# Optimization experiments

Measured on AMD Instinct MI355X. Metric: run time of the kernel, lower is better.

The kernel has to match this reference:

```python
import jax, jax.numpy as jnp
import numpy as np

N_HEAD = 8
D_HEAD = 64
HIDDEN = 512
T = 2048
BS = 4
SCALE = D_HEAD ** -0.5


def setup_inputs() -> dict:
    key = jax.random.key(0)
    k1, k2, k3 = jax.random.split(key, 3)
    x = jax.random.normal(k1, (BS, T, HIDDEN), dtype=jnp.float32)
    # torch Linear weight is (out,in); we store as (in,out) for x @ W
    W_qkv = jax.random.normal(k2, (HIDDEN, (2 * N_HEAD + 1) * D_HEAD), dtype=jnp.float32) * 0.02
    W_out = jax.random.normal(k3, (D_HEAD, HIDDEN), dtype=jnp.float32) * 0.02
    return {"x": x, "W_qkv": W_qkv, "W_out": W_out}


def reference(x, W_qkv, W_out):
    bs, t, h = x.shape
    qkv = x @ W_qkv  # (bs, t, (2H+1)*d)
    q, k, v = jnp.split(qkv, [N_HEAD * D_HEAD, 2 * N_HEAD * D_HEAD], axis=-1)
    q = q.reshape(bs, t, N_HEAD, D_HEAD)
    k = k.reshape(bs, t, N_HEAD, D_HEAD)
    # v is shared across heads: (bs, t, d)
    score = jnp.einsum("bqhd,bkhd->bhqk", q, k) * SCALE
    causal = jnp.triu(jnp.full((t, t), -jnp.inf, dtype=score.dtype), 1)
    score = score + causal[None, None, :, :]
    prob = jax.nn.softmax(score, axis=-1)  # (bs, H, t, t)
    attn_vec = jnp.einsum("bhqk,bkd->bhqd", prob, v)  # shared V broadcast over heads
    m_attn_vec = jnp.mean(attn_vec, axis=1)  # head-mean: (bs, t, d)
    out = m_attn_vec @ W_out  # (bs, t, hidden)
    return out, attn_vec
```

## Files before the change

kernel.cpp:

```cpp
#include <hip/hip_runtime.h>
#include <hip/hip_bf16.h>

#define NHEAD  8
#define DHEAD  64
#define HIDDEN 512
#define SEQ_T  2048
#define BATCH  4
#define NQKV   1088
#define QPITCH 1152
#define NT     32
#define NROWS  (BATCH * SEQ_T)
#define NBH    (BATCH * NHEAD)
#define QSC    (0.125f * 1.44269504f)

typedef __attribute__((ext_vector_type(8))) short short8;
typedef __attribute__((ext_vector_type(4))) float f32x4;

__device__ __forceinline__ unsigned short f2bf(float f) {
  unsigned int u = __float_as_uint(f);
  u += 0x7FFFu + ((u >> 16) & 1u);
  return (unsigned short)(u >> 16);
}
__device__ __forceinline__ float bf2f(unsigned short u) {
  return __uint_as_float((unsigned int)u << 16);
}

__device__ __forceinline__ void load_lds16(const unsigned short* g, unsigned short* l) {
  __builtin_amdgcn_global_load_lds((const __attribute__((address_space(1))) void*)g,
                                   (__attribute__((address_space(3))) void*)l, 16, 0, 0);
}

__global__ __launch_bounds__(256) void prep(const float* __restrict__ x,
                                            const float* __restrict__ W,
                                            const float* __restrict__ Wout,
                                            unsigned short* __restrict__ xb,
                                            unsigned short* __restrict__ Wt,
                                            unsigned short* __restrict__ Wob) {
  const int bx = blockIdx.x;
  const int tid = threadIdx.x;
  if (bx < 2048) {
    const size_t i0 = ((size_t)bx * 256 + tid) * 8;
    float4 a = *(const float4*)(x + i0);
    float4 b = *(const float4*)(x + i0 + 4);
    ushort4 u0, u1;
    u0.x = f2bf(a.x); u0.y = f2bf(a.y); u0.z = f2bf(a.z); u0.w = f2bf(a.w);
    u1.x = f2bf(b.x); u1.y = f2bf(b.y); u1.z = f2bf(b.z); u1.w = f2bf(b.w);
    *(ushort4*)(xb + i0) = u0;
    *(ushort4*)(xb + i0 + 4) = u1;
    return;
  }
  if (bx >= 2184 && bx < 2192) {
    const int z = bx - 2184;
    const size_t base = (size_t)NQKV * HIDDEN + ((size_t)z * 256 + tid) * 16;
    uint4 zero = {0u, 0u, 0u, 0u};
    *(uint4*)(Wt + base) = zero;
    *(uint4*)(Wt + base + 8) = zero;
    return;
  }
  if (bx >= 2192) {
    const int n0 = (bx - 2192) * 64;
    __shared__ float T[64 * 65];
#pragma unroll
    for (int i = 0; i < 4; ++i) {
      int f = tid + i * 256;
      int r = f >> 4;
      int c4 = (f & 15) * 4;
      float4 v = *(const float4*)(Wout + (size_t)r * HIDDEN + n0 + c4);
      T[r * 65 + c4 + 0] = v.x;
      T[r * 65 + c4 + 1] = v.y;
      T[r * 65 + c4 + 2] = v.z;
      T[r * 65 + c4 + 3] = v.w;
    }
    __syncthreads();
#pragma unroll
    for (int i = 0; i < 4; ++i) {
      int f = tid + i * 256;
      int n = f >> 4;
      int k4 = (f & 15) * 4;
      ushort4 u;
      u.x = f2bf(T[(k4 + 0) * 65 + n]);
      u.y = f2bf(T[(k4 + 1) * 65 + n]);
      u.z = f2bf(T[(k4 + 2) * 65 + n]);
      u.w = f2bf(T[(k4 + 3) * 65 + n]);
      *(ushort4*)(Wob + (size_t)(n0 + n) * DHEAD + k4) = u;
    }
    return;
  }
  const int idx = bx - 2048;
  const int n0 = (idx % 17) * 64;
  const int k0 = (idx / 17) * 64;
  __shared__ float T[64 * 65];
#pragma unroll
  for (int i = 0; i < 4; ++i) {
    int f = tid + i * 256;
    int r = f >> 4;
    int c4 = (f & 15) * 4;
    float4 v = *(const float4*)(W + (size_t)(k0 + r) * NQKV + n0 + c4);
    T[r * 65 + c4 + 0] = v.x;
    T[r * 65 + c4 + 1] = v.y;
    T[r * 65 + c4 + 2] = v.z;
    T[r * 65 + c4 + 3] = v.w;
  }
  __syncthreads();
#pragma unroll
  for (int i = 0; i < 4; ++i) {
    int f = tid + i * 256;
    int n = f >> 4;
    int k4 = (f & 15) * 4;
    ushort4 u;
    u.x = f2bf(T[(k4 + 0) * 65 + n]);
    u.y = f2bf(T[(k4 + 1) * 65 + n]);
    u.z = f2bf(T[(k4 + 2) * 65 + n]);
    u.w = f2bf(T[(k4 + 3) * 65 + n]);
    *(ushort4*)(Wt + (size_t)(n0 + n) * HIDDEN + k0 + k4) = u;
  }
}

__global__ __launch_bounds__(256, 3) void qkv_mfma(const unsigned short* __restrict__ Xb,
                                                   const unsigned short* __restrict__ Wt,
                                                   unsigned short* __restrict__ Y,
                                                   unsigned short* __restrict__ vt) {
  __shared__ __align__(16) unsigned short SH[2 * 128 * 64];
  unsigned short* As = SH;
  unsigned short* Bs = SH + 128 * 64;
  const int L = blockIdx.x;
  const int slot = L >> 3;
  const int bm = (L & 7) * 8 + (slot & 7);
  const int bn = slot >> 3;
  const int tid = threadIdx.x;
  const int wave = tid >> 6;
  const int lane = tid & 63;
  const int quad = lane >> 4;
  const int l15 = lane & 15;
  const int lrow = lane >> 3;
  const int lchunk = lane & 7;

  const unsigned short* xrow = Xb + (size_t)bm * 128 * HIDDEN;
  const unsigned short* wrow = Wt + (size_t)bn * 128 * HIDDEN;

  f32x4 acc[2][8];
#pragma unroll
  for (int mt = 0; mt < 2; ++mt)
#pragma unroll
    for (int nt = 0; nt < 8; ++nt) acc[mt][nt] = (f32x4){0.f, 0.f, 0.f, 0.f};

  for (int k0 = 0; k0 < HIDDEN; k0 += 64) {
    __syncthreads();
#pragma unroll
    for (int c = 0; c < 4; ++c) {
      int call = wave * 4 + c;
      int m = call * 8 + lrow;
      int clog = lchunk ^ lrow;
      load_lds16(xrow + (size_t)m * HIDDEN + k0 + clog * 8, &As[call * 512]);
      load_lds16(wrow + (size_t)m * HIDDEN + k0 + clog * 8, &Bs[call * 512]);
    }
    __syncthreads();

#pragma unroll
    for (int ks = 0; ks < 2; ++ks) {
      short8 a[2], b[8];
#pragma unroll
      for (int mt = 0; mt < 2; ++mt) {
        int m = wave * 32 + mt * 16 + l15;
        int phys = (ks * 4 + quad) ^ (l15 & 7);
        a[mt] = *(const short8*)&As[m * 64 + phys * 8];
      }
#pragma unroll
      for (int nt = 0; nt < 8; ++nt) {
        int n = nt * 16 + l15;
        int phys = (ks * 4 + quad) ^ (l15 & 7);
        b[nt] = *(const short8*)&Bs[n * 64 + phys * 8];
      }
#pragma unroll
      for (int mt = 0; mt < 2; ++mt)
#pragma unroll
        for (int nt = 0; nt < 8; ++nt)
          acc[mt][nt] = __builtin_amdgcn_mfma_f32_16x16x32_bf16(a[mt], b[nt], acc[mt][nt], 0, 0, 0);
    }
  }

  if (bn != 8) {
    const float qs = (bn < 4) ? QSC : 1.0f;
#pragma unroll
    for (int mt = 0; mt < 2; ++mt)
#pragma unroll
      for (int r = 0; r < 4; ++r) {
        int row = bm * 128 + wave * 32 + mt * 16 + quad * 4 + r;
#pragma unroll
        for (int nt = 0; nt < 8; ++nt) {
          int col = bn * 128 + nt * 16 + l15;
          Y[(size_t)row * QPITCH + col] = f2bf(acc[mt][nt][r] * qs);
        }
      }
  } else {
    __syncthreads();
    unsigned short* Vs = SH;
#pragma unroll
    for (int mt = 0; mt < 2; ++mt)
#pragma unroll
      for (int nt = 0; nt < 4; ++nt)
#pragma unroll
        for (int r = 0; r < 4; ++r) {
          int lr = wave * 32 + mt * 16 + quad * 4 + r;
          int d = nt * 16 + l15;
          Vs[d * 130 + lr] = f2bf(acc[mt][nt][r]);
        }
    __syncthreads();
    const int bb = bm >> 4;
    const int t0 = (bm & 15) * 128;
    const int half = lane >> 5;
    const int np = lane & 31;
    const int s2 = ((np & 16) << 1) | ((np & 2) << 3) | (np & 12) | ((np & 1) << 1);
#pragma unroll
    for (int i = 0; i < 16; ++i) {
      int d = i * 4 + wave;
      unsigned int v = *(const unsigned int*)&Vs[d * 130 + half * 64 + s2];
      *(unsigned int*)&vt[((size_t)bb * DHEAD + d) * SEQ_T + t0 + half * 64 + 2 * np] = v;
    }
  }
}

__global__ __launch_bounds__(256, 3) void attn_pass(const unsigned short* __restrict__ qkv,
                                                    const unsigned short* __restrict__ vt,
                                                    unsigned short* __restrict__ pbuf0,
                                                    unsigned short* __restrict__ pbuf1,
                                                    float* __restrict__ lbuf) {
  const int bh = blockIdx.x;
  const int y = blockIdx.y;
  const int qt = 15 - (y >> 1);
  const int kh = y & 1;
  const int b = bh >> 3;
  const int h = bh & 7;
  const int tid = threadIdx.x;
  const int wave = tid >> 6;
  const int lane = tid & 63;
  const int quad = lane >> 4;
  const int l15 = lane & 15;

  __shared__ __align__(16) unsigned short Ks[2][64 * 64];
  __shared__ __align__(16) unsigned short Vts[2][64 * 64];

  const unsigned short* bq = qkv + (size_t)b * SEQ_T * QPITCH;
  const unsigned short* bvt = vt + (size_t)b * DHEAD * SEQ_T;

  const int q0 = qt * 128;
  const int kbeg = kh ? (qt + 1) : 0;
  const int kend = kh ? (2 * qt + 1) : qt;

  short8 aq[2][2];
#pragma unroll
  for (int s = 0; s < 2; ++s) {
    const unsigned short* qp = bq + (size_t)(q0 + s * 64 + wave * 16 + l15) * QPITCH + h * 64 + quad * 8;
    aq[s][0] = *(const short8*)qp;
    aq[s][1] = *(const short8*)(qp + 32);
  }

  f32x4 o[2][4];
#pragma unroll
  for (int s = 0; s < 2; ++s)
#pragma unroll
    for (int t = 0; t < 4; ++t) o[s][t] = (f32x4){0.f, 0.f, 0.f, 0.f};
  f32x4 ol[2] = {(f32x4){0.f, 0.f, 0.f, 0.f}, (f32x4){0.f, 0.f, 0.f, 0.f}};
  const short8 vone = {(short)0x3F80, (short)0x3F80, (short)0x3F80, (short)0x3F80,
                       (short)0x3F80, (short)0x3F80, (short)0x3F80, (short)0x3F80};

  const int srow = tid >> 3;
  const int sch = (tid & 7) ^ (srow & 7);
  const int ph0 = (quad ^ (l15 & 7)) * 8;

#pragma unroll
  for (int c = 0; c < 2; ++c) {
    load_lds16(bq + (size_t)(kbeg * 64 + c * 32 + srow) * QPITCH + 512 + h * 64 + sch * 8,
               &Ks[0][c * 2048 + wave * 512]);
    load_lds16(bvt + (size_t)(c * 32 + srow) * SEQ_T + kbeg * 64 + sch * 8,
               &Vts[0][c * 2048 + wave * 512]);
  }

  for (int kt = kbeg; kt <= kend; ++kt) {
    const int k0 = kt * 64;
    const int cur = (kt - kbeg) & 1;
    __syncthreads();
    if (kt < kend) {
      const int kn = (kt + 1) * 64;
      const int nxt = cur ^ 1;
#pragma unroll
      for (int c = 0; c < 2; ++c) {
        load_lds16(bq + (size_t)(kn + c * 32 + srow) * QPITCH + 512 + h * 64 + sch * 8,
                   &Ks[nxt][c * 2048 + wave * 512]);
        load_lds16(bvt + (size_t)(c * 32 + srow) * SEQ_T + kn + sch * 8,
                   &Vts[nxt][c * 2048 + wave * 512]);
      }
    }

    const unsigned short* ksb = Ks[cur];
    const unsigned short* vsb = Vts[cur];
    const bool needMask = (k0 + 63) > q0;

    short8 bk[4][2];
#pragma unroll
    for (int t = 0; t < 4; ++t) {
      const unsigned short* kp = &ksb[(l15 + 16 * t) * 64];
      bk[t][0] = *(const short8*)(kp + ph0);
      bk[t][1] = *(const short8*)(kp + (ph0 ^ 32));
    }

    short8 ap[2][2];
#pragma unroll
    for (int s = 0; s < 2; ++s) {
      f32x4 pr[4];
#pragma unroll
      for (int t = 0; t < 4; ++t) {
        f32x4 sv = (f32x4){0.f, 0.f, 0.f, 0.f};
        sv = __builtin_amdgcn_mfma_f32_16x16x32_bf16(bk[t][0], aq[s][0], sv, 0, 0, 0);
        sv = __builtin_amdgcn_mfma_f32_16x16x32_bf16(bk[t][1], aq[s][1], sv, 0, 0, 0);
        pr[t] = sv;
      }
      const int qrow = q0 + s * 64 + wave * 16 + l15;
#pragma unroll
      for (int t = 0; t < 4; ++t)
#pragma unroll
        for (int r = 0; r < 4; ++r) {
          float p = __builtin_amdgcn_exp2f(pr[t][r]);
          if (needMask)
            p = (k0 + 16 * t + 4 * quad + r <= qrow) ? p : 0.f;
          pr[t][r] = p;
        }
#pragma unroll
      for (int c = 0; c < 2; ++c) {
        union { unsigned int u[4]; short8 v; } pk;
        pk.u[0] = __builtin_amdgcn_perm(__float_as_uint(pr[2 * c][1]),
                                        __float_as_uint(pr[2 * c][0]), 0x07060302u);
        pk.u[1] = __builtin_amdgcn_perm(__float_as_uint(pr[2 * c][3]),
                                        __float_as_uint(pr[2 * c][2]), 0x07060302u);
        pk.u[2] = __builtin_amdgcn_perm(__float_as_uint(pr[2 * c + 1][1]),
                                        __float_as_uint(pr[2 * c + 1][0]), 0x07060302u);
        pk.u[3] = __builtin_amdgcn_perm(__float_as_uint(pr[2 * c + 1][3]),
                                        __float_as_uint(pr[2 * c + 1][2]), 0x07060302u);
        ap[s][c] = pk.v;
      }
      ol[s] = __builtin_amdgcn_mfma_f32_16x16x32_bf16(ap[s][0], vone, ol[s], 0, 0, 0);
      ol[s] = __builtin_amdgcn_mfma_f32_16x16x32_bf16(ap[s][1], vone, ol[s], 0, 0, 0);
    }

    short8 bv[4][2];
#pragma unroll
    for (int t = 0; t < 4; ++t) {
      const unsigned short* vp = &vsb[(l15 + 16 * t) * 64];
      bv[t][0] = *(const short8*)(vp + ph0);
      bv[t][1] = *(const short8*)(vp + (ph0 ^ 32));
    }

#pragma unroll
    for (int t = 0; t < 4; ++t)
#pragma unroll
      for (int s = 0; s < 2; ++s) {
        o[s][t] = __builtin_amdgcn_mfma_f32_16x16x32_bf16(ap[s][0], bv[t][0], o[s][t], 0, 0, 0);
        o[s][t] = __builtin_amdgcn_mfma_f32_16x16x32_bf16(ap[s][1], bv[t][1], o[s][t], 0, 0, 0);
      }
  }

  unsigned short* pb = kh ? pbuf1 : pbuf0;
#pragma unroll
  for (int s = 0; s < 2; ++s) {
#pragma unroll
    for (int r = 0; r < 4; ++r) {
      const int trow = q0 + s * 64 + wave * 16 + quad * 4 + r;
      if (l15 == 0) lbuf[kh * (NBH * SEQ_T) + bh * SEQ_T + trow] = ol[s][r];
      const size_t base = ((size_t)bh * SEQ_T + trow) * DHEAD;
#pragma unroll
      for (int t = 0; t < 4; ++t) pb[base + l15 + 16 * t] = f2bf(o[s][t][r]);
    }
  }
}

__global__ __launch_bounds__(256) void out_merge(const unsigned short* __restrict__ pbuf0,
                                                 const unsigned short* __restrict__ pbuf1,
                                                 const float* __restrict__ lbuf,
                                                 const unsigned short* __restrict__ Wob,
                                                 float* __restrict__ attnv,
                                                 float* __restrict__ out) {
  const int row0 = blockIdx.x * 16;
  const int tid = threadIdx.x;
  __shared__ float Ms[16][66];

  {
    const int lr = tid >> 4;
    const int d0 = (tid & 15) * 4;
    const int row = row0 + lr;
    const int b = row >> 11;
    const int t = row & 2047;
    float s0 = 0.f, s1 = 0.f, s2 = 0.f, s3 = 0.f;
#pragma unroll
    for (int hh = 0; hh < NHEAD; ++hh) {
      const size_t ridx = (size_t)(b * NHEAD + hh) * SEQ_T + t;
      const float inv = 1.0f / (lbuf[ridx] + lbuf[NBH * SEQ_T + ridx]);
      const size_t idx = ridx * DHEAD + d0;
      ushort4 A = *(const ushort4*)(pbuf0 + idx);
      ushort4 B = *(const ushort4*)(pbuf1 + idx);
      float4 m;
      m.x = (bf2f(A.x) + bf2f(B.x)) * inv;
      m.y = (bf2f(A.y) + bf2f(B.y)) * inv;
      m.z = (bf2f(A.z) + bf2f(B.z)) * inv;
      m.w = (bf2f(A.w) + bf2f(B.w)) * inv;
      *(float4*)(attnv + idx) = m;
      s0 += m.x; s1 += m.y; s2 += m.z; s3 += m.w;
    }
    Ms[lr][d0 + 0] = s0 * 0.125f;
    Ms[lr][d0 + 1] = s1 * 0.125f;
    Ms[lr][d0 + 2] = s2 * 0.125f;
    Ms[lr][d0 + 3] = s3 * 0.125f;
  }
  __syncthreads();

  const int wv = tid >> 6;
  const int lane = tid & 63;
  const int quad = lane >> 4;
  const int l15 = lane & 15;

  short8 am[2];
  {
    union { unsigned short us[16]; short8 v[2]; } u;
#pragma unroll
    for (int j = 0; j < 8; ++j) {
      u.us[j] = f2bf(Ms[l15][quad * 8 + j]);
      u.us[8 + j] = f2bf(Ms[l15][32 + quad * 8 + j]);
    }
    am[0] = u.v[0];
    am[1] = u.v[1];
  }

#pragma unroll
  for (int nt = 0; nt < 8; ++nt) {
    const int n = wv * 128 + nt * 16 + l15;
    short8 b0 = *(const short8*)&Wob[(size_t)n * DHEAD + quad * 8];
    short8 b1 = *(const short8*)&Wob[(size_t)n * DHEAD + 32 + quad * 8];
    f32x4 c = (f32x4){0.f, 0.f, 0.f, 0.f};
    c = __builtin_amdgcn_mfma_f32_16x16x32_bf16(am[0], b0, c, 0, 0, 0);
    c = __builtin_amdgcn_mfma_f32_16x16x32_bf16(am[1], b1, c, 0, 0, 0);
#pragma unroll
    for (int r = 0; r < 4; ++r)
      out[(size_t)(row0 + quad * 4 + r) * HIDDEN + n] = c[r];
  }
}

extern "C" void kernel_launch(void* const* d_in, const int* in_sizes, int n_in,
                              void* d_out, int out_size, void* d_ws, size_t ws_size,
                              hipStream_t stream) {
  const float* x     = (const float*)d_in[0];
  const float* W_qkv = (const float*)d_in[1];
  const float* W_out = (const float*)d_in[2];

  float* out      = (float*)d_out;
  float* attn_vec = out + (size_t)BATCH * SEQ_T * HIDDEN;

  unsigned short* qkv  = (unsigned short*)d_ws;
  unsigned short* vt   = qkv + (size_t)NROWS * QPITCH;
  unsigned short* xb   = vt + (size_t)BATCH * DHEAD * SEQ_T;
  unsigned short* Wt   = xb + (size_t)NROWS * HIDDEN;
  unsigned short* pbuf0 = Wt + (size_t)QPITCH * HIDDEN;
  unsigned short* pbuf1 = pbuf0 + (size_t)NBH * SEQ_T * DHEAD;
  float*          lbuf  = (float*)(pbuf1 + (size_t)NBH * SEQ_T * DHEAD);
  unsigned short* Wob   = (unsigned short*)(lbuf + 2 * NBH * SEQ_T);

  prep<<<dim3(2048 + 136 + 8 + 8), 256, 0, stream>>>(x, W_qkv, W_out, xb, Wt, Wob);
  qkv_mfma<<<dim3(576), 256, 0, stream>>>(xb, Wt, qkv, vt);
  attn_pass<<<dim3(NBH, 32), 256, 0, stream>>>(qkv, vt, pbuf0, pbuf1, lbuf);
  out_merge<<<dim3(512), 256, 0, stream>>>(pbuf0, pbuf1, lbuf, Wob, attn_vec, out);
}
```

Baseline: 130.1 us.

## Use 256-row query tiles with variable key-range splits per attention block

Each attention block now covers 256 query rows (four 64-row sub-tiles) instead of 128, so every K/V tile staged in LDS is reused by twice as many query rows. The causal key range of each query tile is split into a variable number of slices (1 to 4), giving 20 blocks per batch-head with roughly balanced work. The partial outputs and row sums go into up to four slice buffers, which out_merge then adds together. Register pressure rises, so occupancy is lowered to 2 waves per SIMD, and the merge step now reads more partial buffers.

```diff
diff --git a/kernel.cpp b/kernel.cpp
--- a/kernel.cpp
+++ b/kernel.cpp
@@ -11,6 +11,8 @@
 #define NT     32
 #define NROWS  (BATCH * SEQ_T)
 #define NBH    (BATCH * NHEAD)
+#define LPITCH (NBH * SEQ_T)
+#define OSLICE ((size_t)NBH * SEQ_T * DHEAD)
 #define QSC    (0.125f * 1.44269504f)
 
 typedef __attribute__((ext_vector_type(8))) short short8;
@@ -220,15 +222,22 @@
   }
 }
 
-__global__ __launch_bounds__(256, 3) void attn_pass(const unsigned short* __restrict__ qkv,
+__global__ __launch_bounds__(256, 2) void attn_pass(const unsigned short* __restrict__ qkv,
                                                     const unsigned short* __restrict__ vt,
-                                                    unsigned short* __restrict__ pbuf0,
-                                                    unsigned short* __restrict__ pbuf1,
+                                                    unsigned short* __restrict__ pbuf,
                                                     float* __restrict__ lbuf) {
   const int bh = blockIdx.x;
-  const int y = blockIdx.y;
-  const int qt = 15 - (y >> 1);
-  const int kh = y & 1;
+  const int yy = 19 - blockIdx.y;
+  const int qt = (yy >= 1) + (yy >= 2) + (yy >= 4) + (yy >= 6) +
+                 (yy >= 9) + (yy >= 12) + (yy >= 16);
+  const int m = qt >> 1;
+  const int Cq = (qt & 1) ? (m + 1) * (m + 1) : m * (m + 1);
+  const int si = yy - Cq;
+  const int ns = m + 1;
+  const int ntile = 4 * qt + 4;
+  const int kbeg = (si * ntile) / ns;
+  const int kend = ((si + 1) * ntile) / ns - 1;
+
   const int b = bh >> 3;
   const int h = bh & 7;
   const int tid = threadIdx.x;
@@ -243,24 +252,24 @@
   const unsigned short* bq = qkv + (size_t)b * SEQ_T * QPITCH;
   const unsigned short* bvt = vt + (size_t)b * DHEAD * SEQ_T;
 
-  const int q0 = qt * 128;
-  const int kbeg = kh ? (qt + 1) : 0;
-  const int kend = kh ? (2 * qt + 1) : qt;
-
-  short8 aq[2][2];
-#pragma unroll
-  for (int s = 0; s < 2; ++s) {
+  const int q0 = qt * 256;
+
+  short8 aq[4][2];
+#pragma unroll
+  for (int s = 0; s < 4; ++s) {
     const unsigned short* qp = bq + (size_t)(q0 + s * 64 + wave * 16 + l15) * QPITCH + h * 64 + quad * 8;
     aq[s][0] = *(const short8*)qp;
     aq[s][1] = *(const short8*)(qp + 32);
   }
 
-  f32x4 o[2][4];
-#pragma unroll
-  for (int s = 0; s < 2; ++s)
+  f32x4 o[4][4];
+#pragma unroll
+  for (int s = 0; s < 4; ++s)
 #pragma unroll
     for (int t = 0; t < 4; ++t) o[s][t] = (f32x4){0.f, 0.f, 0.f, 0.f};
-  f32x4 ol[2] = {(f32x4){0.f, 0.f, 0.f, 0.f}, (f32x4){0.f, 0.f, 0.f, 0.f}};
+  f32x4 ol[4];
+#pragma unroll
+  for (int s = 0; s < 4; ++s) ol[s] = (f32x4){0.f, 0.f, 0.f, 0.f};
   const short8 vone = {(short)0x3F80, (short)0x3F80, (short)0x3F80, (short)0x3F80,
                        (short)0x3F80, (short)0x3F80, (short)0x3F80, (short)0x3F80};
 
@@ -294,19 +303,20 @@
 
     const unsigned short* ksb = Ks[cur];
     const unsigned short* vsb = Vts[cur];
-    const bool needMask = (k0 + 63) > q0;
-
-    short8 bk[4][2];
+
+    short8 bk[4][2], bv[4][2];
 #pragma unroll
     for (int t = 0; t < 4; ++t) {
       const unsigned short* kp = &ksb[(l15 + 16 * t) * 64];
       bk[t][0] = *(const short8*)(kp + ph0);
       bk[t][1] = *(const short8*)(kp + (ph0 ^ 32));
-    }
-
-    short8 ap[2][2];
-#pragma unroll
-    for (int s = 0; s < 2; ++s) {
+      const unsigned short* vp = &vsb[(l15 + 16 * t) * 64];
+      bv[t][0] = *(const short8*)(vp + ph0);
+      bv[t][1] = *(const short8*)(vp + (ph0 ^ 32));
+    }
+
+#pragma unroll
+    for (int s = 0; s < 4; ++s) {
       f32x4 pr[4];
 #pragma unroll
       for (int t = 0; t < 4; ++t) {
@@ -316,6 +326,7 @@
         pr[t] = sv;
       }
       const int qrow = q0 + s * 64 + wave * 16 + l15;
+      const bool needMask = (k0 + 63) > (q0 + s * 64);
 #pragma unroll
       for (int t = 0; t < 4; ++t)
 #pragma unroll
@@ -325,6 +336,7 @@
             p = (k0 + 16 * t + 4 * quad + r <= qrow) ? p : 0.f;
           pr[t][r] = p;
         }
+      short8 ap[2];
 #pragma unroll
       for (int c = 0; c < 2; ++c) {
         union { unsigned int u[4]; short8 v; } pk;
@@ -336,36 +348,25 @@
                                         __float_as_uint(pr[2 * c + 1][0]), 0x07060302u);
         pk.u[3] = __builtin_amdgcn_perm(__float_as_uint(pr[2 * c + 1][3]),
                                         __float_as_uint(pr[2 * c + 1][2]), 0x07060302u);
-        ap[s][c] = pk.v;
-      }
-      ol[s] = __builtin_amdgcn_mfma_f32_16x16x32_bf16(ap[s][0], vone, ol[s], 0, 0, 0);
-      ol[s] = __builtin_amdgcn_mfma_f32_16x16x32_bf16(ap[s][1], vone, ol[s], 0, 0, 0);
-    }
-
-    short8 bv[4][2];
-#pragma unroll
-    for (int t = 0; t < 4; ++t) {
-      const unsigned short* vp = &vsb[(l15 + 16 * t) * 64];
-      bv[t][0] = *(const short8*)(vp + ph0);
-      bv[t][1] = *(const short8*)(vp + (ph0 ^ 32));
-    }
-
-#pragma unroll
-    for (int t = 0; t < 4; ++t)
-#pragma unroll
-      for (int s = 0; s < 2; ++s) {
-        o[s][t] = __builtin_amdgcn_mfma_f32_16x16x32_bf16(ap[s][0], bv[t][0], o[s][t], 0, 0, 0);
-        o[s][t] = __builtin_amdgcn_mfma_f32_16x16x32_bf16(ap[s][1], bv[t][1], o[s][t], 0, 0, 0);
-      }
-  }
-
-  unsigned short* pb = kh ? pbuf1 : pbuf0;
-#pragma unroll
-  for (int s = 0; s < 2; ++s) {
+        ap[c] = pk.v;
+      }
+      ol[s] = __builtin_amdgcn_mfma_f32_16x16x32_bf16(ap[0], vone, ol[s], 0, 0, 0);
+      ol[s] = __builtin_amdgcn_mfma_f32_16x16x32_bf16(ap[1], vone, ol[s], 0, 0, 0);
+#pragma unroll
+      for (int t = 0; t < 4; ++t) {
+        o[s][t] = __builtin_amdgcn_mfma_f32_16x16x32_bf16(ap[0], bv[t][0], o[s][t], 0, 0, 0);
+        o[s][t] = __builtin_amdgcn_mfma_f32_16x16x32_bf16(ap[1], bv[t][1], o[s][t], 0, 0, 0);
+      }
+    }
+  }
+
+  unsigned short* pb = pbuf + (size_t)si * OSLICE;
+#pragma unroll
+  for (int s = 0; s < 4; ++s) {
 #pragma unroll
     for (int r = 0; r < 4; ++r) {
       const int trow = q0 + s * 64 + wave * 16 + quad * 4 + r;
-      if (l15 == 0) lbuf[kh * (NBH * SEQ_T) + bh * SEQ_T + trow] = ol[s][r];
+      if (l15 == 0) lbuf[si * LPITCH + bh * SEQ_T + trow] = ol[s][r];
       const size_t base = ((size_t)bh * SEQ_T + trow) * DHEAD;
 #pragma unroll
       for (int t = 0; t < 4; ++t) pb[base + l15 + 16 * t] = f2bf(o[s][t][r]);
@@ -373,8 +374,7 @@
   }
 }
 
-__global__ __launch_bounds__(256) void out_merge(const unsigned short* __restrict__ pbuf0,
-                                                 const unsigned short* __restrict__ pbuf1,
+__global__ __launch_bounds__(256) void out_merge(const unsigned short* __restrict__ pbuf,
                                                  const float* __restrict__ lbuf,
                                                  const unsigned short* __restrict__ Wob,
                                                  float* __restrict__ attnv,
@@ -389,21 +389,33 @@
     const int row = row0 + lr;
     const int b = row >> 11;
     const int t = row & 2047;
+    const int ns = (t >> 9) + 1;
     float s0 = 0.f, s1 = 0.f, s2 = 0.f, s3 = 0.f;
 #pragma unroll
     for (int hh = 0; hh < NHEAD; ++hh) {
       const size_t ridx = (size_t)(b * NHEAD + hh) * SEQ_T + t;
-      const float inv = 1.0f / (lbuf[ridx] + lbuf[NBH * SEQ_T + ridx]);
+      float l = 0.f;
+      float4 macc = {0.f, 0.f, 0.f, 0.f};
       const size_t idx = ridx * DHEAD + d0;
-      ushort4 A = *(const ushort4*)(pbuf0 + idx);
-      ushort4 B = *(const ushort4*)(pbuf1 + idx);
-      float4 m;
-      m.x = (bf2f(A.x) + bf2f(B.x)) * inv;
-      m.y = (bf2f(A.y) + bf2f(B.y)) * inv;
-      m.z = (bf2f(A.z) + bf2f(B.z)) * inv;
-      m.w = (bf2f(A.w) + bf2f(B.w)) * inv;
-      *(float4*)(attnv + idx) = m;
-      s0 += m.x; s1 += m.y; s2 += m.z; s3 += m.w;
+#pragma unroll
+      for (int si = 0; si < 4; ++si) {
+        if (si < ns) {
+          l += lbuf[si * LPITCH + ridx];
+          ushort4 A = *(const ushort4*)(pbuf + si * OSLICE + idx);
+          macc.x += bf2f(A.x);
+          macc.y += bf2f(A.y);
+          macc.z += bf2f(A.z);
+          macc.w += bf2f(A.w);
+        }
+      }
+      const float inv = 1.0f / l;
+      float4 mv;
+      mv.x = macc.x * inv;
+      mv.y = macc.y * inv;
+      mv.z = macc.z * inv;
+      mv.w = macc.w * inv;
+      *(float4*)(attnv + idx) = mv;
+      s0 += mv.x; s1 += mv.y; s2 += mv.z; s3 += mv.w;
     }
     Ms[lr][d0 + 0] = s0 * 0.125f;
     Ms[lr][d0 + 1] = s1 * 0.125f;
@@ -457,13 +469,12 @@
   unsigned short* vt   = qkv + (size_t)NROWS * QPITCH;
   unsigned short* xb   = vt + (size_t)BATCH * DHEAD * SEQ_T;
   unsigned short* Wt   = xb + (size_t)NROWS * HIDDEN;
-  unsigned short* pbuf0 = Wt + (size_t)QPITCH * HIDDEN;
-  unsigned short* pbuf1 = pbuf0 + (size_t)NBH * SEQ_T * DHEAD;
-  float*          lbuf  = (float*)(pbuf1 + (size_t)NBH * SEQ_T * DHEAD);
-  unsigned short* Wob   = (unsigned short*)(lbuf + 2 * NBH * SEQ_T);
+  unsigned short* pbuf = Wt + (size_t)QPITCH * HIDDEN;
+  float*          lbuf = (float*)(pbuf + 4 * OSLICE);
+  unsigned short* Wob  = (unsigned short*)(lbuf + 4 * LPITCH);
 
   prep<<<dim3(2048 + 136 + 8 + 8), 256, 0, stream>>>(x, W_qkv, W_out, xb, Wt, Wob);
   qkv_mfma<<<dim3(576), 256, 0, stream>>>(xb, Wt, qkv, vt);
-  attn_pass<<<dim3(NBH, 32), 256, 0, stream>>>(qkv, vt, pbuf0, pbuf1, lbuf);
-  out_merge<<<dim3(512), 256, 0, stream>>>(pbuf0, pbuf1, lbuf, Wob, attn_vec, out);
-}
+  attn_pass<<<dim3(NBH, 20), 256, 0, stream>>>(qkv, vt, pbuf, lbuf);
+  out_merge<<<dim3(512), 256, 0, stream>>>(pbuf, lbuf, Wob, attn_vec, out);
+}
```

New measurement: 148.2 us. 1.14x slower.
